# Kernel optimization log

Hardware: AMD Instinct MI355X
Metric: run time of the kernel (lower is better)

The kernel has to match this reference:

```python
import jax, jax.numpy as jnp
import numpy as np

B, L, W, NEG = 128, 80, 5, 5
N, D = 500000, 128
NEG_WEIGHT = 1.0
LAP_NORM = 0.01


def _build_indices():
    # init_emb2pos_index / init_emb2neg_index, vectorized over batch
    posu_w, posv_w = [], []
    for i in range(L):
        for j in range(max(0, i - W), i):
            posu_w.append(j); posv_w.append(i)
        for j in range(i + 1, min(L, i + 1 + W)):
            posu_w.append(j); posv_w.append(i)
    posu_w = np.asarray(posu_w, np.int32)
    posv_w = np.asarray(posv_w, np.int32)
    off = (np.arange(B, dtype=np.int32) * L)[:, None]
    posu = (posu_w[None, :] + off).reshape(-1)
    posv = (posv_w[None, :] + off).reshape(-1)
    negu_w = np.repeat(posv_w, NEG)  # each center index repeated `negative` times
    negu = (negu_w[None, :] + off).reshape(-1)
    pool = np.tile(np.arange(B * L, dtype=np.int32), NEG * W * 2)
    rng = np.random.default_rng(0)
    negv = rng.permutation(pool)[: negu.shape[0]]
    return posu, posv, negu, negv


def setup_inputs() -> dict:
    key = jax.random.key(0)
    k1, k2, k3 = jax.random.split(key, 3)
    initrange = 1.0 / D
    u_weight = jax.random.uniform(k1, (N, D), jnp.float32, -initrange, initrange)
    # original inits v to zeros; use small random values for a nontrivial test
    v_weight = jax.random.normal(k2, (N, D), jnp.float32) * 0.01
    nodes = jax.random.randint(k3, (B, L), 0, N, jnp.int32)
    posu, posv, negu, negv = _build_indices()
    return {
        "u_weight": u_weight,
        "v_weight": v_weight,
        "nodes": nodes,
        "index_emb_posu": jnp.asarray(posu),
        "index_emb_posv": jnp.asarray(posv),
        "index_emb_negu": jnp.asarray(negu),
        "index_emb_negv": jnp.asarray(negv),
    }


def _sigmoid_lut():
    t = jax.nn.sigmoid(jnp.arange(-6.01, 6.01, 0.01, dtype=jnp.float32))
    return t.at[0].set(0.0).at[-1].set(1.0)


def _lut_sigmoid(table, score):
    score = jnp.clip(score, -6.0, 6.0)
    idx = jnp.clip(jnp.floor((score + 6.01) / 0.01).astype(jnp.int32), 0, table.shape[0] - 1)
    return table[idx]


def reference(u_weight, v_weight, nodes, index_emb_posu, index_emb_posv,
              index_emb_negu, index_emb_negv):
    BL = nodes.shape[0] * nodes.shape[1]
    table = _sigmoid_lut()
    flat = nodes.reshape(-1)
    emb_u = u_weight[flat]  # [BL, D]
    emb_v = v_weight[flat]  # [BL, D]

    # positive pairs
    emb_pos_u = emb_u[index_emb_posu]
    emb_pos_v = emb_v[index_emb_posv]
    pos_score = jnp.sum(emb_pos_u * emb_pos_v, axis=1)
    s_pos = (1.0 - _lut_sigmoid(table, pos_score))[:, None]
    grad_u_pos = s_pos * emb_pos_v + LAP_NORM * (emb_pos_v - emb_pos_u)
    grad_v_pos = s_pos * emb_pos_u + LAP_NORM * (emb_pos_u - emb_pos_v)
    grad_u = jax.ops.segment_sum(grad_u_pos, index_emb_posu, num_segments=BL)
    grad_v = jax.ops.segment_sum(grad_v_pos, index_emb_posv, num_segments=BL)

    # negative pairs
    emb_neg_u = emb_u[index_emb_negu]
    emb_neg_v = emb_v[index_emb_negv]
    neg_score = jnp.sum(emb_neg_u * emb_neg_v, axis=1)
    s_neg = (-_lut_sigmoid(table, neg_score))[:, None]
    grad_u = grad_u + jax.ops.segment_sum(NEG_WEIGHT * s_neg * emb_neg_v,
                                          index_emb_negu, num_segments=BL)
    grad_v = grad_v + jax.ops.segment_sum(NEG_WEIGHT * s_neg * emb_neg_u,
                                          index_emb_negv, num_segments=BL)
    return grad_u, grad_v
```

## Files before the change

### kernel.cpp

```cpp
#include <hip/hip_runtime.h>

#define DD  128
#define LL  80
#define WW  5
#define NEGS 5
#define EW  64

__device__ __forceinline__ int degf(int i) {
    return (i < WW ? i : WW) + ((LL - 1 - i) < WW ? (LL - 1 - i) : WW);
}
__device__ __forceinline__ int prefixf(int i) {
    if (i <= WW) return WW * i + i * (i - 1) / 2;
    if (i <= LL - WW) return 35 + 10 * (i - WW);
    int e = 735;
    for (int t = LL - WW; t < i; ++t) e += (LL + WW - 1) - t;
    return e;
}

__device__ __forceinline__ float qsig(float p) {
    float s = fminf(fmaxf(p, -6.0f), 6.0f);
    int idx = (int)floorf((s + 6.01f) / 0.01f);
    idx = idx < 0 ? 0 : (idx > 1201 ? 1201 : idx);
    float t = fmaf((float)idx, 0.01f, -6.01f);
    float sig = 1.0f / (1.0f + __expf(-t));
    return idx <= 0 ? 0.0f : (idx >= 1201 ? 1.0f : sig);
}

__global__ void k_prep(const float* __restrict__ uw, const float* __restrict__ vw,
                       const int* __restrict__ nodes,
                       const int* __restrict__ nu, const int* __restrict__ nv,
                       int BL, int NP, int G_g,
                       float* __restrict__ eu, float* __restrict__ ev,
                       int* __restrict__ cnt, unsigned short* __restrict__ ell) {
    int b = blockIdx.x;
    int t = threadIdx.x;
    if (b < G_g) {
        int r = b * 8 + (t >> 5);
        if (r >= BL) return;
        int l = t & 31;
        long n = (long)nodes[r];
        ((float4*)(eu + (long)r * DD))[l] = ((const float4*)(uw + n * DD))[l];
        ((float4*)(ev + (long)r * DD))[l] = ((const float4*)(vw + n * DD))[l];
    } else {
        int p = (b - G_g) * blockDim.x + t;
        if (p < NP) {
            int vr = nv[p];
            int ur = nu[p];
            int s = atomicAdd(&cnt[vr], 1);
            if (s < EW) ell[(long)vr * EW + s] = (unsigned short)ur;
        }
    }
}

__global__ __launch_bounds__(256) void k_grad(const float* __restrict__ eu,
                                              const float* __restrict__ ev,
                                              const int* __restrict__ cnt,
                                              const unsigned short* __restrict__ ell,
                                              const int* __restrict__ negv,
                                              float* __restrict__ out,
                                              int BL, int ppb) {
    int lane = threadIdx.x & 63;
    int row = blockIdx.x * 4 + (threadIdx.x >> 6);
    if (row >= 2 * BL) return;

    bool is_u = row < BL;
    int r = is_u ? row : row - BL;
    int bb = r / LL;
    int i  = r - bb * LL;
    const float* own = is_u ? eu : ev;
    const float* oth = is_u ? ev : eu;

    int li  = lane & 15;
    int sub = lane >> 4;

    const float4* orow = (const float4*)(own + (long)r * DD);
    float4 o0 = orow[li * 2 + 0];
    float4 o1 = orow[li * 2 + 1];

    float4 a0 = make_float4(0.f, 0.f, 0.f, 0.f);
    float4 a1 = make_float4(0.f, 0.f, 0.f, 0.f);

    int nlo = i < WW ? i : WW;
    int deg = degf(i);
    int base = bb * LL;

#define PAIR_STEP(x0_, x1_, cpos_, valid_)                                   \
    {                                                                        \
        float p_ = o0.x * (x0_).x;                                           \
        p_ = fmaf(o0.y, (x0_).y, p_); p_ = fmaf(o0.z, (x0_).z, p_);          \
        p_ = fmaf(o0.w, (x0_).w, p_); p_ = fmaf(o1.x, (x1_).x, p_);          \
        p_ = fmaf(o1.y, (x1_).y, p_); p_ = fmaf(o1.z, (x1_).z, p_);          \
        p_ = fmaf(o1.w, (x1_).w, p_);                                        \
        p_ += __shfl_xor(p_, 1, 16); p_ += __shfl_xor(p_, 2, 16);            \
        p_ += __shfl_xor(p_, 4, 16); p_ += __shfl_xor(p_, 8, 16);            \
        float c_ = (cpos_ ? 1.01f : 0.0f) - qsig(p_);                        \
        c_ = (valid_) ? c_ : 0.0f;                                           \
        a0.x = fmaf(c_, (x0_).x, a0.x); a0.y = fmaf(c_, (x0_).y, a0.y);      \
        a0.z = fmaf(c_, (x0_).z, a0.z); a0.w = fmaf(c_, (x0_).w, a0.w);      \
        a1.x = fmaf(c_, (x1_).x, a1.x); a1.y = fmaf(c_, (x1_).y, a1.y);      \
        a1.z = fmaf(c_, (x1_).z, a1.z); a1.w = fmaf(c_, (x1_).w, a1.w);      \
    }

    for (int k = 0; k < deg; k += 4) {
        int t0 = k + sub;
        int tc = t0 < deg - 1 ? t0 : deg - 1;
        int j = (tc < nlo) ? (i - nlo + tc) : (i + 1 + tc - nlo);
        const float4* xr = (const float4*)(oth + (long)(base + j) * DD);
        float4 x0 = xr[li * 2 + 0];
        float4 x1 = xr[li * 2 + 1];
        PAIR_STEP(x0, x1, true, t0 < deg);
    }

    if (is_u) {
        int pb = bb * ppb + NEGS * prefixf(i);
        int nn = NEGS * deg;
        int last = nn - 1;
        int e0 = negv[pb + (sub < last ? sub : last)];
        int e1 = negv[pb + (4 + sub < last ? 4 + sub : last)];
        const float4* xr = (const float4*)(oth + (long)e0 * DD);
        float4 x0 = xr[li * 2 + 0];
        float4 x1 = xr[li * 2 + 1];
        for (int k = 0; k < nn; k += 4) {
            const float4* xrn = (const float4*)(oth + (long)e1 * DD);
            float4 nx0 = xrn[li * 2 + 0];
            float4 nx1 = xrn[li * 2 + 1];
            int ki = k + 8 + sub; ki = ki < last ? ki : last;
            int e2 = negv[pb + ki];
            PAIR_STEP(x0, x1, false, (k + sub) < nn);
            e1 = e2; x0 = nx0; x1 = nx1;
        }
    } else {
        int nn = cnt[r]; nn = nn > EW ? EW : nn;
        if (nn > 0) {
            const unsigned short* lst = ell + (long)r * EW;
            int last = nn - 1;
            int e0 = (int)lst[sub < last ? sub : last];
            int e1 = (int)lst[4 + sub < last ? 4 + sub : last];
            const float4* xr = (const float4*)(oth + (long)e0 * DD);
            float4 x0 = xr[li * 2 + 0];
            float4 x1 = xr[li * 2 + 1];
            for (int k = 0; k < nn; k += 4) {
                const float4* xrn = (const float4*)(oth + (long)e1 * DD);
                float4 nx0 = xrn[li * 2 + 0];
                float4 nx1 = xrn[li * 2 + 1];
                int ki = k + 8 + sub; ki = ki < last ? ki : last;
                int e2 = (int)lst[ki];
                PAIR_STEP(x0, x1, false, (k + sub) < nn);
                e1 = e2; x0 = nx0; x1 = nx1;
            }
        }
    }
#undef PAIR_STEP

#define XRED(v) v += __shfl_xor(v, 16, 64); v += __shfl_xor(v, 32, 64)
    XRED(a0.x); XRED(a0.y); XRED(a0.z); XRED(a0.w);
    XRED(a1.x); XRED(a1.y); XRED(a1.z); XRED(a1.w);
#undef XRED

    float lam = -0.01f * (float)deg;
    a0.x = fmaf(lam, o0.x, a0.x); a0.y = fmaf(lam, o0.y, a0.y);
    a0.z = fmaf(lam, o0.z, a0.z); a0.w = fmaf(lam, o0.w, a0.w);
    a1.x = fmaf(lam, o1.x, a1.x); a1.y = fmaf(lam, o1.y, a1.y);
    a1.z = fmaf(lam, o1.z, a1.z); a1.w = fmaf(lam, o1.w, a1.w);

    if (sub == 0) {
        float4* od = (float4*)(out + (long)row * DD);
        od[li * 2 + 0] = a0;
        od[li * 2 + 1] = a1;
    }
}

extern "C" void kernel_launch(void* const* d_in, const int* in_sizes, int n_in,
                              void* d_out, int out_size, void* d_ws, size_t ws_size,
                              hipStream_t stream) {
    const float* uw  = (const float*)d_in[0];
    const float* vw  = (const float*)d_in[1];
    const int* nodes = (const int*)d_in[2];
    const int* nu    = (const int*)d_in[5];
    const int* nv    = (const int*)d_in[6];
    int BL = in_sizes[2];
    int NP = in_sizes[5];
    float* out = (float*)d_out;

    int B   = BL / LL;
    int ppb = NP / B;

    float* eu = (float*)d_ws;
    float* ev = eu + (size_t)BL * DD;
    int* cnt  = (int*)(ev + (size_t)BL * DD);
    unsigned short* ell = (unsigned short*)(cnt + (size_t)BL);

    hipMemsetAsync(cnt, 0, (size_t)BL * sizeof(int), stream);

    int G_g = (BL + 7) / 8;
    int G_b = (NP + 255) / 256;
    k_prep<<<G_g + G_b, 256, 0, stream>>>(uw, vw, nodes, nu, nv,
                                          BL, NP, G_g, eu, ev, cnt, ell);

    int rows = 2 * BL;
    k_grad<<<(rows + 3) / 4, 256, 0, stream>>>(eu, ev, cnt, ell, nv, out, BL, ppb);
}
```

Before: 92.89 us.

## Drop staged embedding copies; gather rows directly from weight tables via node indices

Removes the prep-stage copy of the gathered u/v embedding rows into workspace. The prep kernel now stores translated node ids, both the neighbour node ids in the ELL lists (widened to 32-bit) and the negative-target node ids, and the grad kernel reads rows straight from the large weight tables. This avoids writing and re-reading about 10 MB of staged embeddings, at the cost of scattered reads from a 256 MB table with less cache locality and an extra index indirection per positive pair. The LUT sigmoid also changes to multiply by 100 instead of dividing by 0.01 and uses a hardware reciprocal, which could shift floor results at bin edges.

```diff
diff --git a/kernel.cpp b/kernel.cpp
--- a/kernel.cpp
+++ b/kernel.cpp
@@ -19,44 +19,35 @@
 
 __device__ __forceinline__ float qsig(float p) {
     float s = fminf(fmaxf(p, -6.0f), 6.0f);
-    int idx = (int)floorf((s + 6.01f) / 0.01f);
-    idx = idx < 0 ? 0 : (idx > 1201 ? 1201 : idx);
-    float t = fmaf((float)idx, 0.01f, -6.01f);
-    float sig = 1.0f / (1.0f + __expf(-t));
-    return idx <= 0 ? 0.0f : (idx >= 1201 ? 1.0f : sig);
+    float fi = floorf((s + 6.01f) * 100.0f);
+    int idx = (int)fi;
+    float t = fmaf(fi, 0.01f, -6.01f);
+    float sig = __builtin_amdgcn_rcpf(1.0f + __expf(-t));
+    sig = idx <= 0 ? 0.0f : (idx >= 1201 ? 1.0f : sig);
+    return sig;
 }
 
-__global__ void k_prep(const float* __restrict__ uw, const float* __restrict__ vw,
-                       const int* __restrict__ nodes,
+__global__ void k_prep(const int* __restrict__ nodes,
                        const int* __restrict__ nu, const int* __restrict__ nv,
-                       int BL, int NP, int G_g,
-                       float* __restrict__ eu, float* __restrict__ ev,
-                       int* __restrict__ cnt, unsigned short* __restrict__ ell) {
-    int b = blockIdx.x;
-    int t = threadIdx.x;
-    if (b < G_g) {
-        int r = b * 8 + (t >> 5);
-        if (r >= BL) return;
-        int l = t & 31;
-        long n = (long)nodes[r];
-        ((float4*)(eu + (long)r * DD))[l] = ((const float4*)(uw + n * DD))[l];
-        ((float4*)(ev + (long)r * DD))[l] = ((const float4*)(vw + n * DD))[l];
-    } else {
-        int p = (b - G_g) * blockDim.x + t;
-        if (p < NP) {
-            int vr = nv[p];
-            int ur = nu[p];
-            int s = atomicAdd(&cnt[vr], 1);
-            if (s < EW) ell[(long)vr * EW + s] = (unsigned short)ur;
-        }
-    }
+                       int NP,
+                       int* __restrict__ cnt, unsigned* __restrict__ ell,
+                       int* __restrict__ nvnode) {
+    int p = blockIdx.x * blockDim.x + threadIdx.x;
+    if (p >= NP) return;
+    int vr = nv[p];
+    int ur = nu[p];
+    int un = nodes[ur];
+    nvnode[p] = nodes[vr];
+    int s = atomicAdd(&cnt[vr], 1);
+    if (s < EW) ell[(long)vr * EW + s] = (unsigned)un;
 }
 
-__global__ __launch_bounds__(256) void k_grad(const float* __restrict__ eu,
-                                              const float* __restrict__ ev,
+__global__ __launch_bounds__(256) void k_grad(const float* __restrict__ uw,
+                                              const float* __restrict__ vw,
+                                              const int* __restrict__ nodes,
                                               const int* __restrict__ cnt,
-                                              const unsigned short* __restrict__ ell,
-                                              const int* __restrict__ negv,
+                                              const unsigned* __restrict__ ell,
+                                              const int* __restrict__ nvnode,
                                               float* __restrict__ out,
                                               int BL, int ppb) {
     int lane = threadIdx.x & 63;
@@ -67,13 +58,14 @@
     int r = is_u ? row : row - BL;
     int bb = r / LL;
     int i  = r - bb * LL;
-    const float* own = is_u ? eu : ev;
-    const float* oth = is_u ? ev : eu;
+    const float* ownw = is_u ? uw : vw;
+    const float* othw = is_u ? vw : uw;
 
     int li  = lane & 15;
     int sub = lane >> 4;
 
-    const float4* orow = (const float4*)(own + (long)r * DD);
+    long onode = (long)nodes[r];
+    const float4* orow = (const float4*)(ownw + onode * DD);
     float4 o0 = orow[li * 2 + 0];
     float4 o1 = orow[li * 2 + 1];
 
@@ -105,7 +97,8 @@
         int t0 = k + sub;
         int tc = t0 < deg - 1 ? t0 : deg - 1;
         int j = (tc < nlo) ? (i - nlo + tc) : (i + 1 + tc - nlo);
-        const float4* xr = (const float4*)(oth + (long)(base + j) * DD);
+        long pn = (long)nodes[base + j];
+        const float4* xr = (const float4*)(othw + pn * DD);
         float4 x0 = xr[li * 2 + 0];
         float4 x1 = xr[li * 2 + 1];
         PAIR_STEP(x0, x1, true, t0 < deg);
@@ -115,36 +108,36 @@
         int pb = bb * ppb + NEGS * prefixf(i);
         int nn = NEGS * deg;
         int last = nn - 1;
-        int e0 = negv[pb + (sub < last ? sub : last)];
-        int e1 = negv[pb + (4 + sub < last ? 4 + sub : last)];
-        const float4* xr = (const float4*)(oth + (long)e0 * DD);
+        long e0 = (long)nvnode[pb + (sub < last ? sub : last)];
+        long e1 = (long)nvnode[pb + (4 + sub < last ? 4 + sub : last)];
+        const float4* xr = (const float4*)(othw + e0 * DD);
         float4 x0 = xr[li * 2 + 0];
         float4 x1 = xr[li * 2 + 1];
         for (int k = 0; k < nn; k += 4) {
-            const float4* xrn = (const float4*)(oth + (long)e1 * DD);
+            const float4* xrn = (const float4*)(othw + e1 * DD);
             float4 nx0 = xrn[li * 2 + 0];
             float4 nx1 = xrn[li * 2 + 1];
             int ki = k + 8 + sub; ki = ki < last ? ki : last;
-            int e2 = negv[pb + ki];
+            long e2 = (long)nvnode[pb + ki];
             PAIR_STEP(x0, x1, false, (k + sub) < nn);
             e1 = e2; x0 = nx0; x1 = nx1;
         }
     } else {
         int nn = cnt[r]; nn = nn > EW ? EW : nn;
         if (nn > 0) {
-            const unsigned short* lst = ell + (long)r * EW;
+            const unsigned* lst = ell + (long)r * EW;
             int last = nn - 1;
-            int e0 = (int)lst[sub < last ? sub : last];
-            int e1 = (int)lst[4 + sub < last ? 4 + sub : last];
-            const float4* xr = (const float4*)(oth + (long)e0 * DD);
+            long e0 = (long)lst[sub < last ? sub : last];
+            long e1 = (long)lst[4 + sub < last ? 4 + sub : last];
+            const float4* xr = (const float4*)(othw + e0 * DD);
             float4 x0 = xr[li * 2 + 0];
             float4 x1 = xr[li * 2 + 1];
             for (int k = 0; k < nn; k += 4) {
-                const float4* xrn = (const float4*)(oth + (long)e1 * DD);
+                const float4* xrn = (const float4*)(othw + e1 * DD);
                 float4 nx0 = xrn[li * 2 + 0];
                 float4 nx1 = xrn[li * 2 + 1];
                 int ki = k + 8 + sub; ki = ki < last ? ki : last;
-                int e2 = (int)lst[ki];
+                long e2 = (long)lst[ki];
                 PAIR_STEP(x0, x1, false, (k + sub) < nn);
                 e1 = e2; x0 = nx0; x1 = nx1;
             }
@@ -185,18 +178,16 @@
     int B   = BL / LL;
     int ppb = NP / B;
 
-    float* eu = (float*)d_ws;
-    float* ev = eu + (size_t)BL * DD;
-    int* cnt  = (int*)(ev + (size_t)BL * DD);
-    unsigned short* ell = (unsigned short*)(cnt + (size_t)BL);
+    int* cnt = (int*)d_ws;
+    unsigned* ell = (unsigned*)(cnt + (size_t)BL);
+    int* nvnode = (int*)(ell + (size_t)BL * EW);
 
     hipMemsetAsync(cnt, 0, (size_t)BL * sizeof(int), stream);
 
-    int G_g = (BL + 7) / 8;
-    int G_b = (NP + 255) / 256;
-    k_prep<<<G_g + G_b, 256, 0, stream>>>(uw, vw, nodes, nu, nv,
-                                          BL, NP, G_g, eu, ev, cnt, ell);
+    k_prep<<<(NP + 255) / 256, 256, 0, stream>>>(nodes, nu, nv, NP,
+                                                 cnt, ell, nvnode);
 
     int rows = 2 * BL;
-    k_grad<<<(rows + 3) / 4, 256, 0, stream>>>(eu, ev, cnt, ell, nv, out, BL, ppb);
+    k_grad<<<(rows + 3) / 4, 256, 0, stream>>>(uw, vw, nodes, cnt, ell,
+                                               nvnode, out, BL, ppb);
 }
```

After: 93.10 us. About the same (+0.2%).
